# Kernel optimization log

Measured on AMD Instinct MI355X. Metric: run time of the kernel, lower is better.

## Reference

```python
import jax, jax.numpy as jnp
import numpy as np

N_NODES = 32768
N_EDGES = 65536
NODE_IN = 4
EDGE_IN = 4
HIDDEN = 64
LN_EPS = 1e-5


def setup_inputs() -> dict:
    key = jax.random.key(0)
    ks = jax.random.split(key, 20)
    s = 0.05
    inp = {
        "x": jax.random.normal(ks[0], (N_NODES, NODE_IN), dtype=jnp.float32),
        "edge_attr": jax.random.normal(ks[1], (N_EDGES, EDGE_IN), dtype=jnp.float32),
        "edge_index": jax.random.randint(ks[2], (2, N_EDGES), 0, N_NODES, dtype=jnp.int64),
        "batch": jnp.zeros((N_NODES,), dtype=jnp.int64),
        # layer 1: edge MLP edge_in->64->node_in*hidden, root [node_in,hidden]
        "e1_w1": jax.random.normal(ks[3], (EDGE_IN, 64), dtype=jnp.float32) * s,
        "e1_b1": jnp.zeros((64,), jnp.float32),
        "e1_w2": jax.random.normal(ks[4], (64, NODE_IN * HIDDEN), dtype=jnp.float32) * s,
        "e1_b2": jnp.zeros((NODE_IN * HIDDEN,), jnp.float32),
        "root1": jax.random.normal(ks[5], (NODE_IN, HIDDEN), dtype=jnp.float32) * s,
        "bias1": jnp.zeros((HIDDEN,), jnp.float32),
        "ln1_g": jnp.ones((HIDDEN,), jnp.float32),
        "ln1_b": jnp.zeros((HIDDEN,), jnp.float32),
        # layer 2: edge MLP edge_in->128->hidden*hidden, root [hidden,hidden]
        "e2_w1": jax.random.normal(ks[6], (EDGE_IN, 128), dtype=jnp.float32) * s,
        "e2_b1": jnp.zeros((128,), jnp.float32),
        "e2_w2": jax.random.normal(ks[7], (128, HIDDEN * HIDDEN), dtype=jnp.float32) * s,
        "e2_b2": jnp.zeros((HIDDEN * HIDDEN,), jnp.float32),
        "root2": jax.random.normal(ks[8], (HIDDEN, HIDDEN), dtype=jnp.float32) * s,
        "bias2": jnp.zeros((HIDDEN,), jnp.float32),
        "ln2_g": jnp.ones((HIDDEN,), jnp.float32),
        "ln2_b": jnp.zeros((HIDDEN,), jnp.float32),
    }
    return inp


def _nnconv(x, src, dst, edge_attr, ew1, eb1, ew2, eb2, root, bias, n_nodes):
    # edge-conditioned weights: [E, in_ch, out_ch]
    in_ch = x.shape[1]
    out_ch = root.shape[1]
    h = jax.nn.relu(edge_attr @ ew1 + eb1) @ ew2 + eb2
    W = h.reshape(-1, in_ch, out_ch)
    # gather source features, per-edge matvec, scatter-mean to dest
    msg = jnp.einsum('ei,eio->eo', x[src], W)  # [E, out_ch]
    summed = jax.ops.segment_sum(msg, dst, num_segments=n_nodes)
    cnt = jax.ops.segment_sum(jnp.ones((dst.shape[0],), msg.dtype), dst,
                              num_segments=n_nodes)
    agg = summed / jnp.maximum(cnt, 1.0)[:, None]
    return agg + x @ root + bias


def _layernorm(x, g, b):
    m = x.mean(-1, keepdims=True)
    v = ((x - m) ** 2).mean(-1, keepdims=True)
    return (x - m) * jax.lax.rsqrt(v + LN_EPS) * g + b


def reference(x, edge_attr, e1_w1, e1_b1, e1_w2, e1_b2, root1, bias1, ln1_g, ln1_b,
              e2_w1, e2_b1, e2_w2, e2_b2, root2, bias2, ln2_g, ln2_b,
              edge_index, batch):
    src, dst = edge_index[0], edge_index[1]
    n = x.shape[0]
    h = _nnconv(x, src, dst, edge_attr, e1_w1, e1_b1, e1_w2, e1_b2, root1, bias1, n)
    h = _layernorm(jax.nn.relu(h), ln1_g, ln1_b)  # dropout = identity (eval)
    h = _nnconv(h, src, dst, edge_attr, e2_w1, e2_b1, e2_w2, e2_b2, root2, bias2, n)
    h = _layernorm(jax.nn.relu(h), ln2_g, ln2_b)
    # global mean pool (single graph -> [1, hidden])
    gs = jax.ops.segment_sum(h, batch, num_segments=1)
    gc = jax.ops.segment_sum(jnp.ones((n,), h.dtype), batch, num_segments=1)
    return gs / jnp.maximum(gc, 1.0)[:, None]
```

## Files before the change

### kernel.cpp

```cpp
#include <hip/hip_runtime.h>

#define N_NODES 32768
#define N_EDGES 65536

typedef float f32x4 __attribute__((ext_vector_type(4)));
typedef short s16x8 __attribute__((ext_vector_type(8)));

__device__ __forceinline__ unsigned short f2bf(float f){
  unsigned u = __float_as_uint(f);
  u += 0x7FFFu + ((u >> 16) & 1u);
  return (unsigned short)(u >> 16);
}
__device__ __forceinline__ float bf2f(unsigned short b){
  return __uint_as_float(((unsigned)b) << 16);
}

__global__ void k_prep(const float* __restrict__ e2_w2, const float* __restrict__ e2_b2,
                       const float* __restrict__ e1_w2,
                       unsigned short* __restrict__ W2f, unsigned short* __restrict__ T1g,
                       int* __restrict__ cz){
  int idx = blockIdx.x * 256 + threadIdx.x;
  if (idx < 129 * 4096){
    int j = idx & 7, l = (idx >> 3) & 63, half = (idx >> 9) & 1, ot = (idx >> 10) & 3, kf = idx >> 12;
    int i = half * 32 + ((l >> 4) << 3) + j;
    int o = ot * 16 + (l & 15);
    float v = (kf < 128) ? e2_w2[kf * 4096 + i * 64 + o] : e2_b2[i * 64 + o];
    W2f[idx] = f2bf(v);
  } else if (idx < 129 * 4096 + 16384){
    int t = idx - 129 * 4096;
    int j = t & 7, l = (t >> 3) & 63, half = (t >> 9) & 1, ot = (t >> 10) & 3, i = t >> 12;
    int kf = half * 32 + ((l >> 4) << 3) + j;
    int o = ot * 16 + (l & 15);
    T1g[t] = f2bf(e1_w2[kf * 256 + i * 64 + o]);
  } else {
    int z = idx - (129 * 4096 + 16384);
    if (z < 65536) cz[z] = 0;
  }
}

__global__ void k_hist(const int* __restrict__ ei, int* __restrict__ cnti){
  int i = blockIdx.x * 256 + threadIdx.x;
  if (i < N_EDGES) atomicAdd(cnti + ei[N_EDGES + i], 1);
}

__global__ void k_scanA(const int* __restrict__ cnti, int* __restrict__ lex, int* __restrict__ bsum){
  const int tid = threadIdx.x;
  int n = blockIdx.x * 256 + tid;
  int c = cnti[n];
  int v = c;
  int lane = tid & 63;
  #pragma unroll
  for (int d = 1; d < 64; d <<= 1){
    int t = __shfl_up(v, d);
    if (lane >= d) v += t;
  }
  __shared__ int wsum[4];
  if (lane == 63) wsum[tid >> 6] = v;
  __syncthreads();
  int off = 0;
  for (int i = 0; i < (tid >> 6); ++i) off += wsum[i];
  lex[n] = off + v - c;
  if (tid == 255) bsum[blockIdx.x] = off + v;
}

__global__ void k_scanB(const int* __restrict__ bsum, int* __restrict__ bsx){
  const int tid = threadIdx.x;
  int c = bsum[tid];
  int v = c;
  int lane = tid & 63;
  #pragma unroll
  for (int d = 1; d < 64; d <<= 1){
    int t = __shfl_up(v, d);
    if (lane >= d) v += t;
  }
  __shared__ int w0;
  if (tid == 63) w0 = v;
  __syncthreads();
  if (tid >= 64) v += w0;
  bsx[tid] = v - c;
}

__global__ void k_fill(const int* __restrict__ ei, const int* __restrict__ lex,
                       const int* __restrict__ bsx, int* __restrict__ cur,
                       int* __restrict__ eslot){
  int e = blockIdx.x * 256 + threadIdx.x;
  if (e < N_EDGES){
    int d = ei[N_EDGES + e];
    int base = lex[d] + bsx[d >> 8];
    eslot[e] = base + atomicAdd(cur + d, 1);
  }
}

__launch_bounds__(256, 4)
__global__ void k_msg1(const float* __restrict__ x, const float* __restrict__ ea,
                       const int* __restrict__ ei, const int* __restrict__ eslot,
                       const float* __restrict__ e1_w1, const float* __restrict__ e1_b1,
                       const float* __restrict__ e1_b2,
                       const unsigned short* __restrict__ T1g,
                       float* __restrict__ msg)
{
  __shared__ float eas[64 * 4];
  __shared__ unsigned short F1f[8 * 64 * 8];
  const int tid = threadIdx.x;
  const int eblk = blockIdx.x * 64;

  if (tid < 64) ((float4*)eas)[tid] = ((const float4*)ea)[eblk + tid];
  __syncthreads();
  {
    int kf = tid & 63, eh = tid >> 6;
    float w0 = e1_w1[kf], w1 = e1_w1[64 + kf], w2 = e1_w1[128 + kf], w3 = e1_w1[192 + kf];
    float bb = e1_b1[kf];
    int half = kf >> 5, hi = (kf >> 3) & 3, j = kf & 7;
    for (int e = eh * 16; e < eh * 16 + 16; ++e){
      float s = fmaf(eas[e*4+0], w0, fmaf(eas[e*4+1], w1, fmaf(eas[e*4+2], w2, fmaf(eas[e*4+3], w3, bb))));
      F1f[(((e >> 4) * 2 + half) * 64 + hi * 16 + (e & 15)) * 8 + j] = f2bf(fmaxf(s, 0.f));
    }
  }
  __syncthreads();

  const int l = tid & 63, lm = l & 15, lg = l >> 4;
  const int ot = tid >> 6;
  int esl[4];
  float xs[4][4];
  s16x8 bf[4][2];
  #pragma unroll
  for (int et = 0; et < 4; ++et){
    int e = eblk + et * 16 + lm;
    int s = ei[e];
    esl[et] = eslot[e];
    float4 xv = *(const float4*)(x + s * 4);
    xs[et][0] = xv.x; xs[et][1] = xv.y; xs[et][2] = xv.z; xs[et][3] = xv.w;
    bf[et][0] = ((const s16x8*)F1f)[(et * 2 + 0) * 64 + l];
    bf[et][1] = ((const s16x8*)F1f)[(et * 2 + 1) * 64 + l];
  }
  f32x4 acc[4];
  #pragma unroll
  for (int et = 0; et < 4; ++et) acc[et] = (f32x4){0.f, 0.f, 0.f, 0.f};

  #pragma unroll
  for (int i = 0; i < 4; ++i){
    const s16x8* p = (const s16x8*)(T1g + (i * 4 + ot) * 1024);
    s16x8 a0 = p[l], a1 = p[64 + l];
    #pragma unroll
    for (int et = 0; et < 4; ++et){
      f32x4 g = (f32x4){0.f, 0.f, 0.f, 0.f};
      g = __builtin_amdgcn_mfma_f32_16x16x32_bf16(a0, bf[et][0], g, 0, 0, 0);
      g = __builtin_amdgcn_mfma_f32_16x16x32_bf16(a1, bf[et][1], g, 0, 0, 0);
      acc[et] += xs[et][i] * g;
    }
  }
  float b2v[4][4];
  #pragma unroll
  for (int i = 0; i < 4; ++i)
    #pragma unroll
    for (int r = 0; r < 4; ++r) b2v[i][r] = e1_b2[i * 64 + ot * 16 + lg * 4 + r];
  #pragma unroll
  for (int et = 0; et < 4; ++et)
    #pragma unroll
    for (int r = 0; r < 4; ++r)
      #pragma unroll
      for (int i = 0; i < 4; ++i) acc[et][r] = fmaf(xs[et][i], b2v[i][r], acc[et][r]);

  #pragma unroll
  for (int et = 0; et < 4; ++et)
    *(f32x4*)(msg + (size_t)esl[et] * 64 + ot * 16 + lg * 4) = acc[et];
}

__launch_bounds__(256)
__global__ void k_node1(const float* __restrict__ x, const float* __restrict__ root1,
                        const float* __restrict__ bias1, const float* __restrict__ lng,
                        const float* __restrict__ lnb, const int* __restrict__ cnti,
                        const int* __restrict__ lex, const int* __restrict__ bsx,
                        const float* __restrict__ msg, unsigned short* __restrict__ h1b)
{
  const int tid = threadIdx.x;
  int n = blockIdx.x * 4 + (tid >> 6);
  int o = tid & 63;
  int rp = lex[n] + bsx[n >> 8];
  int deg = cnti[n];
  float s = 0.f;
  for (int j = 0; j < deg; ++j) s += msg[(size_t)(rp + j) * 64 + o];
  float v = s * (1.f / fmaxf((float)deg, 1.f));
  float4 xv = *(const float4*)(x + n * 4);
  v = fmaf(xv.x, root1[o], v);
  v = fmaf(xv.y, root1[64 + o], v);
  v = fmaf(xv.z, root1[128 + o], v);
  v = fmaf(xv.w, root1[192 + o], v);
  v = fmaxf(v + bias1[o], 0.f);
  float m = v;
  #pragma unroll
  for (int d = 32; d > 0; d >>= 1) m += __shfl_xor(m, d);
  m *= (1.f / 64.f);
  float dd = v - m;
  float var = dd * dd;
  #pragma unroll
  for (int d = 32; d > 0; d >>= 1) var += __shfl_xor(var, d);
  var *= (1.f / 64.f);
  float out = dd * rsqrtf(var + 1e-5f) * lng[o] + lnb[o];
  h1b[n * 64 + o] = f2bf(out);
}

__launch_bounds__(512, 4)
__global__ void k_msg2(const float* __restrict__ ea, const int* __restrict__ ei,
                       const int* __restrict__ eslot,
                       const float* __restrict__ e2_w1, const float* __restrict__ e2_b1,
                       const unsigned short* __restrict__ h1b,
                       const unsigned short* __restrict__ W2f,
                       float* __restrict__ msg)
{
  __shared__ float eas[128 * 4];
  __shared__ float F2s[128 * 132];
  const int tid = threadIdx.x;
  const int eblk = blockIdx.x * 128;
  const int w = tid >> 6, l = tid & 63, lm = l & 15, lg = l >> 4;
  const int ot = w >> 1, eh = w & 1;

  int esl[4];
  s16x8 bh[4][2];
  #pragma unroll
  for (int et = 0; et < 4; ++et){
    int eloc = eh * 64 + et * 16 + lm;
    int e = eblk + eloc;
    int s = ei[e];
    esl[et] = eslot[e];
    const s16x8* hp = (const s16x8*)(h1b + s * 64);
    bh[et][0] = hp[lg];
    bh[et][1] = hp[4 + lg];
  }

  if (tid < 128) ((float4*)eas)[tid] = ((const float4*)ea)[eblk + tid];
  __syncthreads();
  {
    int kf = tid & 127, q = tid >> 7;
    float w0 = e2_w1[kf], w1 = e2_w1[128 + kf], w2 = e2_w1[256 + kf], w3 = e2_w1[384 + kf];
    float bb = e2_b1[kf];
    for (int e = q * 32; e < q * 32 + 32; ++e){
      float s = fmaf(eas[e*4+0], w0, fmaf(eas[e*4+1], w1, fmaf(eas[e*4+2], w2, fmaf(eas[e*4+3], w3, bb))));
      F2s[e * 132 + kf] = fmaxf(s, 0.f);
    }
  }
  __syncthreads();

  f32x4 acc[4];
  #pragma unroll
  for (int et = 0; et < 4; ++et) acc[et] = (f32x4){0.f, 0.f, 0.f, 0.f};

  const int voff = ot * 2048 + l * 16;
  s16x8 A0[2], A1[2], A2[2], A3[2];

#define LOADA(DST, KF) { \
    const unsigned short* sb = W2f + (size_t)(KF) * 4096; \
    asm volatile("global_load_dwordx4 %0, %2, %3\n\t" \
                 "global_load_dwordx4 %1, %2, %3 offset:1024" \
      : "=&v"(DST[0]), "=&v"(DST[1]) : "v"(voff), "s"(sb)); }
#define WAITA(N) do { asm volatile("s_waitcnt vmcnt(" #N ")"); \
                      __builtin_amdgcn_sched_barrier(0); } while(0);
#define STEP(A, J) { \
    _Pragma("unroll") \
    for (int et = 0; et < 4; ++et){ \
      f32x4 g = (f32x4){0.f, 0.f, 0.f, 0.f}; \
      g = __builtin_amdgcn_mfma_f32_16x16x32_bf16(A[0], bh[et][0], g, 0, 0, 0); \
      g = __builtin_amdgcn_mfma_f32_16x16x32_bf16(A[1], bh[et][1], g, 0, 0, 0); \
      acc[et] += f2c[et][J] * g; \
    } }

  LOADA(A0, 0)
  LOADA(A1, 1)
  LOADA(A2, 2)
  LOADA(A3, 3)
  #pragma unroll 1
  for (int kf = 0; kf < 128; kf += 4){
    f32x4 f2c[4];
    #pragma unroll
    for (int et = 0; et < 4; ++et)
      f2c[et] = *(const f32x4*)&F2s[(eh * 64 + et * 16 + lm) * 132 + kf];
    const int k5 = (kf + 5 > 128) ? 128 : kf + 5;
    const int k6 = (kf + 6 > 128) ? 128 : kf + 6;
    const int k7 = (kf + 7 > 128) ? 128 : kf + 7;
    WAITA(6) STEP(A0, 0) LOADA(A0, kf + 4)
    WAITA(6) STEP(A1, 1) LOADA(A1, k5)
    WAITA(6) STEP(A2, 2) LOADA(A2, k6)
    WAITA(6) STEP(A3, 3) LOADA(A3, k7)
  }
  WAITA(0)
  #pragma unroll
  for (int et = 0; et < 4; ++et){
    acc[et] = __builtin_amdgcn_mfma_f32_16x16x32_bf16(A0[0], bh[et][0], acc[et], 0, 0, 0);
    acc[et] = __builtin_amdgcn_mfma_f32_16x16x32_bf16(A0[1], bh[et][1], acc[et], 0, 0, 0);
  }
#undef LOADA
#undef WAITA
#undef STEP

  #pragma unroll
  for (int et = 0; et < 4; ++et)
    *(f32x4*)(msg + (size_t)esl[et] * 64 + ot * 16 + lg * 4) = acc[et];
}

__launch_bounds__(1024)
__global__ void k_node2(const unsigned short* __restrict__ h1b, const float* __restrict__ root2,
                        const float* __restrict__ bias2, const float* __restrict__ lng,
                        const float* __restrict__ lnb, const int* __restrict__ cnti,
                        const int* __restrict__ lex, const int* __restrict__ bsx,
                        const float* __restrict__ msg, float* __restrict__ partial)
{
  const int tid = threadIdx.x;
  const int q = tid >> 6, o = tid & 63;
  float tsum = 0.f;
  #pragma unroll 1
  for (int it = 0; it < 4; ++it){
    int n = blockIdx.x * 64 + it * 16 + q;
    int rp = lex[n] + bsx[n >> 8];
    int deg = cnti[n];
    float s = 0.f;
    for (int j = 0; j < deg; ++j) s += msg[(size_t)(rp + j) * 64 + o];
    float v = s * (1.f / fmaxf((float)deg, 1.f));
    const s16x8* hp = (const s16x8*)(h1b + n * 64);
    #pragma unroll
    for (int c = 0; c < 8; ++c){
      s16x8 hv = hp[c];
      #pragma unroll
      for (int j = 0; j < 8; ++j)
        v = fmaf(bf2f((unsigned short)hv[j]), root2[(c * 8 + j) * 64 + o], v);
    }
    v = fmaxf(v + bias2[o], 0.f);
    float m = v;
    #pragma unroll
    for (int d = 32; d > 0; d >>= 1) m += __shfl_xor(m, d);
    m *= (1.f / 64.f);
    float dd = v - m;
    float var = dd * dd;
    #pragma unroll
    for (int d = 32; d > 0; d >>= 1) var += __shfl_xor(var, d);
    var *= (1.f / 64.f);
    tsum += dd * rsqrtf(var + 1e-5f) * lng[o] + lnb[o];
  }
  __shared__ float pp[16][64];
  pp[q][o] = tsum;
  __syncthreads();
  if (tid < 64){
    float t = 0.f;
    #pragma unroll
    for (int k = 0; k < 16; ++k) t += pp[k][tid];
    partial[blockIdx.x * 64 + tid] = t;
  }
}

__launch_bounds__(1024)
__global__ void k_out(const float* __restrict__ partial, float* __restrict__ out){
  const int tid = threadIdx.x;
  int o = tid & 63, q = tid >> 6;
  float s = 0.f;
  for (int b = q; b < 512; b += 16) s += partial[b * 64 + o];
  __shared__ float pp[16][64];
  pp[q][o] = s;
  __syncthreads();
  if (tid < 64){
    float t = 0.f;
    #pragma unroll
    for (int k = 0; k < 16; ++k) t += pp[k][tid];
    out[tid] = t * (1.f / 32768.f);
  }
}

extern "C" void kernel_launch(void* const* d_in, const int* in_sizes, int n_in,
                              void* d_out, int out_size, void* d_ws, size_t ws_size,
                              hipStream_t stream)
{
  const float* x      = (const float*)d_in[0];
  const float* ea     = (const float*)d_in[1];
  const int*   ei     = (const int*)  d_in[2];
  const float* e1_w1  = (const float*)d_in[4];
  const float* e1_b1  = (const float*)d_in[5];
  const float* e1_w2  = (const float*)d_in[6];
  const float* e1_b2  = (const float*)d_in[7];
  const float* root1  = (const float*)d_in[8];
  const float* bias1  = (const float*)d_in[9];
  const float* ln1g   = (const float*)d_in[10];
  const float* ln1b   = (const float*)d_in[11];
  const float* e2_w1  = (const float*)d_in[12];
  const float* e2_b1  = (const float*)d_in[13];
  const float* e2_w2  = (const float*)d_in[14];
  const float* e2_b2  = (const float*)d_in[15];
  const float* root2  = (const float*)d_in[16];
  const float* bias2  = (const float*)d_in[17];
  const float* ln2g   = (const float*)d_in[18];
  const float* ln2b   = (const float*)d_in[19];

  char* w = (char*)d_ws;
  float*          msg     = (float*)(w);
  unsigned short* h1b     = (unsigned short*)(w + 16777216);
  unsigned short* W2f     = (unsigned short*)(w + 20971520);
  unsigned short* T1g     = (unsigned short*)(w + 22028288);
  int*            cnti    = (int*)(w + 22061056);
  int*            cur     = (int*)(w + 22192128);
  int*            lex     = (int*)(w + 22323200);
  int*            bsx     = (int*)(w + 22454272);
  int*            bsum    = (int*)(w + 22454784);
  int*            eslot   = (int*)(w + 22455296);
  float*          partial = (float*)(w + 22717440);

  k_prep <<<2384, 256, 0, stream>>>(e2_w2, e2_b2, e1_w2, W2f, T1g, cnti);
  k_hist <<<256, 256, 0, stream>>>(ei, cnti);
  k_scanA<<<128, 256, 0, stream>>>(cnti, lex, bsum);
  k_scanB<<<1, 128, 0, stream>>>(bsum, bsx);
  k_fill <<<256, 256, 0, stream>>>(ei, lex, bsx, cur, eslot);
  k_msg1 <<<1024, 256, 0, stream>>>(x, ea, ei, eslot, e1_w1, e1_b1, e1_b2, T1g, msg);
  k_node1<<<8192, 256, 0, stream>>>(x, root1, bias1, ln1g, ln1b, cnti, lex, bsx, msg, h1b);
  k_msg2 <<<512, 512, 0, stream>>>(ea, ei, eslot, e2_w1, e2_b1, h1b, W2f, msg);
  k_node2<<<512, 1024, 0, stream>>>(h1b, root2, bias2, ln2g, ln2b, cnti, lex, bsx, msg, partial);
  k_out  <<<1, 1024, 0, stream>>>(partial, (float*)d_out);
}
```

Before: 156.0 us.

## Split K across waves in msg2 and store layer-1 messages as bf16

After: 171.7 us. 1.1x slower.

```diff
diff --git a/kernel.cpp b/kernel.cpp
--- a/kernel.cpp
+++ b/kernel.cpp
@@ -5,6 +5,7 @@
 
 typedef float f32x4 __attribute__((ext_vector_type(4)));
 typedef short s16x8 __attribute__((ext_vector_type(8)));
+typedef short s16x4 __attribute__((ext_vector_type(4)));
 
 __device__ __forceinline__ unsigned short f2bf(float f){
   unsigned u = __float_as_uint(f);
@@ -97,7 +98,7 @@
                        const float* __restrict__ e1_w1, const float* __restrict__ e1_b1,
                        const float* __restrict__ e1_b2,
                        const unsigned short* __restrict__ T1g,
-                       float* __restrict__ msg)
+                       unsigned short* __restrict__ msg1b)
 {
   __shared__ float eas[64 * 4];
   __shared__ unsigned short F1f[8 * 64 * 8];
@@ -162,8 +163,11 @@
       for (int i = 0; i < 4; ++i) acc[et][r] = fmaf(xs[et][i], b2v[i][r], acc[et][r]);
 
   #pragma unroll
-  for (int et = 0; et < 4; ++et)
-    *(f32x4*)(msg + (size_t)esl[et] * 64 + ot * 16 + lg * 4) = acc[et];
+  for (int et = 0; et < 4; ++et){
+    unsigned p0 = ((unsigned)f2bf(acc[et][1]) << 16) | f2bf(acc[et][0]);
+    unsigned p1 = ((unsigned)f2bf(acc[et][3]) << 16) | f2bf(acc[et][2]);
+    *(uint2*)(msg1b + (size_t)esl[et] * 64 + ot * 16 + lg * 4) = make_uint2(p0, p1);
+  }
 }
 
 __launch_bounds__(256)
@@ -171,7 +175,7 @@
                         const float* __restrict__ bias1, const float* __restrict__ lng,
                         const float* __restrict__ lnb, const int* __restrict__ cnti,
                         const int* __restrict__ lex, const int* __restrict__ bsx,
-                        const float* __restrict__ msg, unsigned short* __restrict__ h1b)
+                        const unsigned short* __restrict__ msg1b, unsigned short* __restrict__ h1b)
 {
   const int tid = threadIdx.x;
   int n = blockIdx.x * 4 + (tid >> 6);
@@ -179,7 +183,7 @@
   int rp = lex[n] + bsx[n >> 8];
   int deg = cnti[n];
   float s = 0.f;
-  for (int j = 0; j < deg; ++j) s += msg[(size_t)(rp + j) * 64 + o];
+  for (int j = 0; j < deg; ++j) s += bf2f(msg1b[(size_t)(rp + j) * 64 + o]);
   float v = s * (1.f / fmaxf((float)deg, 1.f));
   float4 xv = *(const float4*)(x + n * 4);
   v = fmaf(xv.x, root1[o], v);
@@ -209,23 +213,20 @@
                        float* __restrict__ msg)
 {
   __shared__ float eas[128 * 4];
-  __shared__ float F2s[128 * 132];
+  __shared__ __align__(16) unsigned short F2s[128 * 132];
   const int tid = threadIdx.x;
   const int eblk = blockIdx.x * 128;
   const int w = tid >> 6, l = tid & 63, lm = l & 15, lg = l >> 4;
-  const int ot = w >> 1, eh = w & 1;
-
-  int esl[4];
-  s16x8 bh[4][2];
-  #pragma unroll
-  for (int et = 0; et < 4; ++et){
-    int eloc = eh * 64 + et * 16 + lm;
-    int e = eblk + eloc;
+  const int ot = w >> 1, ki = w & 1;
+
+  int esl[8];
+  s16x8 bh[8];
+  #pragma unroll
+  for (int et = 0; et < 8; ++et){
+    int e = eblk + et * 16 + lm;
     int s = ei[e];
     esl[et] = eslot[e];
-    const s16x8* hp = (const s16x8*)(h1b + s * 64);
-    bh[et][0] = hp[lg];
-    bh[et][1] = hp[4 + lg];
+    bh[et] = ((const s16x8*)(h1b + s * 64))[ki * 4 + lg];
   }
 
   if (tid < 128) ((float4*)eas)[tid] = ((const float4*)ea)[eblk + tid];
@@ -236,32 +237,30 @@
     float bb = e2_b1[kf];
     for (int e = q * 32; e < q * 32 + 32; ++e){
       float s = fmaf(eas[e*4+0], w0, fmaf(eas[e*4+1], w1, fmaf(eas[e*4+2], w2, fmaf(eas[e*4+3], w3, bb))));
-      F2s[e * 132 + kf] = fmaxf(s, 0.f);
+      F2s[e * 132 + kf] = f2bf(fmaxf(s, 0.f));
     }
   }
   __syncthreads();
 
-  f32x4 acc[4];
-  #pragma unroll
-  for (int et = 0; et < 4; ++et) acc[et] = (f32x4){0.f, 0.f, 0.f, 0.f};
-
-  const int voff = ot * 2048 + l * 16;
-  s16x8 A0[2], A1[2], A2[2], A3[2];
+  f32x4 acc[8];
+  #pragma unroll
+  for (int et = 0; et < 8; ++et) acc[et] = (f32x4){0.f, 0.f, 0.f, 0.f};
+
+  const int voff = ot * 2048 + ki * 1024 + l * 16;
+  s16x8 A0, A1, A2, A3;
 
 #define LOADA(DST, KF) { \
     const unsigned short* sb = W2f + (size_t)(KF) * 4096; \
-    asm volatile("global_load_dwordx4 %0, %2, %3\n\t" \
-                 "global_load_dwordx4 %1, %2, %3 offset:1024" \
-      : "=&v"(DST[0]), "=&v"(DST[1]) : "v"(voff), "s"(sb)); }
+    asm volatile("global_load_dwordx4 %0, %1, %2" \
+      : "=&v"(DST) : "v"(voff), "s"(sb)); }
 #define WAITA(N) do { asm volatile("s_waitcnt vmcnt(" #N ")"); \
                       __builtin_amdgcn_sched_barrier(0); } while(0);
 #define STEP(A, J) { \
     _Pragma("unroll") \
-    for (int et = 0; et < 4; ++et){ \
+    for (int et = 0; et < 8; ++et){ \
       f32x4 g = (f32x4){0.f, 0.f, 0.f, 0.f}; \
-      g = __builtin_amdgcn_mfma_f32_16x16x32_bf16(A[0], bh[et][0], g, 0, 0, 0); \
-      g = __builtin_amdgcn_mfma_f32_16x16x32_bf16(A[1], bh[et][1], g, 0, 0, 0); \
-      acc[et] += f2c[et][J] * g; \
+      g = __builtin_amdgcn_mfma_f32_16x16x32_bf16(A, bh[et], g, 0, 0, 0); \
+      acc[et] += bf2f((unsigned short)f2c[et][J]) * g; \
     } }
 
   LOADA(A0, 0)
@@ -270,31 +269,41 @@
   LOADA(A3, 3)
   #pragma unroll 1
   for (int kf = 0; kf < 128; kf += 4){
-    f32x4 f2c[4];
-    #pragma unroll
-    for (int et = 0; et < 4; ++et)
-      f2c[et] = *(const f32x4*)&F2s[(eh * 64 + et * 16 + lm) * 132 + kf];
+    s16x4 f2c[8];
+    #pragma unroll
+    for (int et = 0; et < 8; ++et)
+      f2c[et] = *(const s16x4*)&F2s[(et * 16 + lm) * 132 + kf];
     const int k5 = (kf + 5 > 128) ? 128 : kf + 5;
     const int k6 = (kf + 6 > 128) ? 128 : kf + 6;
     const int k7 = (kf + 7 > 128) ? 128 : kf + 7;
-    WAITA(6) STEP(A0, 0) LOADA(A0, kf + 4)
-    WAITA(6) STEP(A1, 1) LOADA(A1, k5)
-    WAITA(6) STEP(A2, 2) LOADA(A2, k6)
-    WAITA(6) STEP(A3, 3) LOADA(A3, k7)
+    WAITA(3) STEP(A0, 0) LOADA(A0, kf + 4)
+    WAITA(3) STEP(A1, 1) LOADA(A1, k5)
+    WAITA(3) STEP(A2, 2) LOADA(A2, k6)
+    WAITA(3) STEP(A3, 3) LOADA(A3, k7)
   }
   WAITA(0)
   #pragma unroll
-  for (int et = 0; et < 4; ++et){
-    acc[et] = __builtin_amdgcn_mfma_f32_16x16x32_bf16(A0[0], bh[et][0], acc[et], 0, 0, 0);
-    acc[et] = __builtin_amdgcn_mfma_f32_16x16x32_bf16(A0[1], bh[et][1], acc[et], 0, 0, 0);
-  }
+  for (int et = 0; et < 8; ++et)
+    acc[et] = __builtin_amdgcn_mfma_f32_16x16x32_bf16(A0, bh[et], acc[et], 0, 0, 0);
 #undef LOADA
 #undef WAITA
 #undef STEP
 
-  #pragma unroll
-  for (int et = 0; et < 4; ++et)
-    *(f32x4*)(msg + (size_t)esl[et] * 64 + ot * 16 + lg * 4) = acc[et];
+  __syncthreads();
+  float* red = (float*)F2s;
+  if (ki == 1){
+    #pragma unroll
+    for (int et = 0; et < 8; ++et)
+      *(f32x4*)&red[((ot * 8 + et) * 64 + l) * 4] = acc[et];
+  }
+  __syncthreads();
+  if (ki == 0){
+    #pragma unroll
+    for (int et = 0; et < 8; ++et){
+      acc[et] += *(const f32x4*)&red[((ot * 8 + et) * 64 + l) * 4];
+      *(f32x4*)(msg + (size_t)esl[et] * 64 + ot * 16 + lg * 4) = acc[et];
+    }
+  }
 }
 
 __launch_bounds__(1024)
@@ -389,6 +398,7 @@
 
   char* w = (char*)d_ws;
   float*          msg     = (float*)(w);
+  unsigned short* msg1b   = (unsigned short*)(w);
   unsigned short* h1b     = (unsigned short*)(w + 16777216);
   unsigned short* W2f     = (unsigned short*)(w + 20971520);
   unsigned short* T1g     = (unsigned short*)(w + 22028288);
@@ -405,8 +415,8 @@
   k_scanA<<<128, 256, 0, stream>>>(cnti, lex, bsum);
   k_scanB<<<1, 128, 0, stream>>>(bsum, bsx);
   k_fill <<<256, 256, 0, stream>>>(ei, lex, bsx, cur, eslot);
-  k_msg1 <<<1024, 256, 0, stream>>>(x, ea, ei, eslot, e1_w1, e1_b1, e1_b2, T1g, msg);
-  k_node1<<<8192, 256, 0, stream>>>(x, root1, bias1, ln1g, ln1b, cnti, lex, bsx, msg, h1b);
+  k_msg1 <<<1024, 256, 0, stream>>>(x, ea, ei, eslot, e1_w1, e1_b1, e1_b2, T1g, msg1b);
+  k_node1<<<8192, 256, 0, stream>>>(x, root1, bias1, ln1g, ln1b, cnti, lex, bsx, msg1b, h1b);
   k_msg2 <<<512, 512, 0, stream>>>(ea, ei, eslot, e2_w1, e2_b1, h1b, W2f, msg);
   k_node2<<<512, 1024, 0, stream>>>(h1b, root2, bias2, ln2g, ln2b, cnti, lex, bsx, msg, partial);
   k_out  <<<1, 1024, 0, stream>>>(partial, (float*)d_out);
```

## Store edge messages in bf16, stage weight prep through LDS, raise MFMA priority

Applied to the files above, without the earlier changes.

New measurement: 155.2 us. Within noise of the previous version (-0.5%).

```diff
diff --git a/kernel.cpp b/kernel.cpp
--- a/kernel.cpp
+++ b/kernel.cpp
@@ -19,21 +19,29 @@
                        const float* __restrict__ e1_w2,
                        unsigned short* __restrict__ W2f, unsigned short* __restrict__ T1g,
                        int* __restrict__ cz){
-  int idx = blockIdx.x * 256 + threadIdx.x;
-  if (idx < 129 * 4096){
-    int j = idx & 7, l = (idx >> 3) & 63, half = (idx >> 9) & 1, ot = (idx >> 10) & 3, kf = idx >> 12;
-    int i = half * 32 + ((l >> 4) << 3) + j;
-    int o = ot * 16 + (l & 15);
-    float v = (kf < 128) ? e2_w2[kf * 4096 + i * 64 + o] : e2_b2[i * 64 + o];
-    W2f[idx] = f2bf(v);
-  } else if (idx < 129 * 4096 + 16384){
-    int t = idx - 129 * 4096;
+  __shared__ float S[4096];
+  const int b = blockIdx.x, tid = threadIdx.x;
+  if (b < 129){
+    const float* src = (b < 128) ? (e2_w2 + b * 4096) : e2_b2;
+    #pragma unroll
+    for (int t = 0; t < 4096; t += 256) S[t + tid] = src[t + tid];
+    __syncthreads();
+    #pragma unroll
+    for (int t = 0; t < 4096; t += 256){
+      int u = t + tid;
+      int j = u & 7, l = (u >> 3) & 63, half = (u >> 9) & 1, ot = (u >> 10) & 3;
+      int i = half * 32 + ((l >> 4) << 3) + j;
+      int o = ot * 16 + (l & 15);
+      W2f[b * 4096 + u] = f2bf(S[i * 64 + o]);
+    }
+  } else if (b < 193){
+    int t = (b - 129) * 256 + tid;
     int j = t & 7, l = (t >> 3) & 63, half = (t >> 9) & 1, ot = (t >> 10) & 3, i = t >> 12;
     int kf = half * 32 + ((l >> 4) << 3) + j;
     int o = ot * 16 + (l & 15);
     T1g[t] = f2bf(e1_w2[kf * 256 + i * 64 + o]);
   } else {
-    int z = idx - (129 * 4096 + 16384);
+    int z = (b - 193) * 256 + tid;
     if (z < 65536) cz[z] = 0;
   }
 }
@@ -97,7 +105,7 @@
                        const float* __restrict__ e1_w1, const float* __restrict__ e1_b1,
                        const float* __restrict__ e1_b2,
                        const unsigned short* __restrict__ T1g,
-                       float* __restrict__ msg)
+                       unsigned short* __restrict__ msg1b)
 {
   __shared__ float eas[64 * 4];
   __shared__ unsigned short F1f[8 * 64 * 8];
@@ -162,8 +170,11 @@
       for (int i = 0; i < 4; ++i) acc[et][r] = fmaf(xs[et][i], b2v[i][r], acc[et][r]);
 
   #pragma unroll
-  for (int et = 0; et < 4; ++et)
-    *(f32x4*)(msg + (size_t)esl[et] * 64 + ot * 16 + lg * 4) = acc[et];
+  for (int et = 0; et < 4; ++et){
+    unsigned p0 = ((unsigned)f2bf(acc[et][1]) << 16) | f2bf(acc[et][0]);
+    unsigned p1 = ((unsigned)f2bf(acc[et][3]) << 16) | f2bf(acc[et][2]);
+    *(uint2*)(msg1b + (size_t)esl[et] * 64 + ot * 16 + lg * 4) = make_uint2(p0, p1);
+  }
 }
 
 __launch_bounds__(256)
@@ -171,7 +182,7 @@
                         const float* __restrict__ bias1, const float* __restrict__ lng,
                         const float* __restrict__ lnb, const int* __restrict__ cnti,
                         const int* __restrict__ lex, const int* __restrict__ bsx,
-                        const float* __restrict__ msg, unsigned short* __restrict__ h1b)
+                        const unsigned short* __restrict__ msg1b, unsigned short* __restrict__ h1b)
 {
   const int tid = threadIdx.x;
   int n = blockIdx.x * 4 + (tid >> 6);
@@ -179,7 +190,7 @@
   int rp = lex[n] + bsx[n >> 8];
   int deg = cnti[n];
   float s = 0.f;
-  for (int j = 0; j < deg; ++j) s += msg[(size_t)(rp + j) * 64 + o];
+  for (int j = 0; j < deg; ++j) s += bf2f(msg1b[(size_t)(rp + j) * 64 + o]);
   float v = s * (1.f / fmaxf((float)deg, 1.f));
   float4 xv = *(const float4*)(x + n * 4);
   v = fmaf(xv.x, root1[o], v);
@@ -206,7 +217,7 @@
                        const float* __restrict__ e2_w1, const float* __restrict__ e2_b1,
                        const unsigned short* __restrict__ h1b,
                        const unsigned short* __restrict__ W2f,
-                       float* __restrict__ msg)
+                       unsigned short* __restrict__ msgb)
 {
   __shared__ float eas[128 * 4];
   __shared__ float F2s[128 * 132];
@@ -256,13 +267,15 @@
 #define WAITA(N) do { asm volatile("s_waitcnt vmcnt(" #N ")"); \
                       __builtin_amdgcn_sched_barrier(0); } while(0);
 #define STEP(A, J) { \
+    __builtin_amdgcn_s_setprio(1); \
     _Pragma("unroll") \
     for (int et = 0; et < 4; ++et){ \
       f32x4 g = (f32x4){0.f, 0.f, 0.f, 0.f}; \
       g = __builtin_amdgcn_mfma_f32_16x16x32_bf16(A[0], bh[et][0], g, 0, 0, 0); \
       g = __builtin_amdgcn_mfma_f32_16x16x32_bf16(A[1], bh[et][1], g, 0, 0, 0); \
       acc[et] += f2c[et][J] * g; \
-    } }
+    } \
+    __builtin_amdgcn_s_setprio(0); }
 
   LOADA(A0, 0)
   LOADA(A1, 1)
@@ -293,8 +306,11 @@
 #undef STEP
 
   #pragma unroll
-  for (int et = 0; et < 4; ++et)
-    *(f32x4*)(msg + (size_t)esl[et] * 64 + ot * 16 + lg * 4) = acc[et];
+  for (int et = 0; et < 4; ++et){
+    unsigned p0 = ((unsigned)f2bf(acc[et][1]) << 16) | f2bf(acc[et][0]);
+    unsigned p1 = ((unsigned)f2bf(acc[et][3]) << 16) | f2bf(acc[et][2]);
+    *(uint2*)(msgb + (size_t)esl[et] * 64 + ot * 16 + lg * 4) = make_uint2(p0, p1);
+  }
 }
 
 __launch_bounds__(1024)
@@ -302,7 +318,7 @@
                         const float* __restrict__ bias2, const float* __restrict__ lng,
                         const float* __restrict__ lnb, const int* __restrict__ cnti,
                         const int* __restrict__ lex, const int* __restrict__ bsx,
-                        const float* __restrict__ msg, float* __restrict__ partial)
+                        const unsigned short* __restrict__ msgb, float* __restrict__ partial)
 {
   const int tid = threadIdx.x;
   const int q = tid >> 6, o = tid & 63;
@@ -313,7 +329,7 @@
     int rp = lex[n] + bsx[n >> 8];
     int deg = cnti[n];
     float s = 0.f;
-    for (int j = 0; j < deg; ++j) s += msg[(size_t)(rp + j) * 64 + o];
+    for (int j = 0; j < deg; ++j) s += bf2f(msgb[(size_t)(rp + j) * 64 + o]);
     float v = s * (1.f / fmaxf((float)deg, 1.f));
     const s16x8* hp = (const s16x8*)(h1b + n * 64);
     #pragma unroll
@@ -388,26 +404,26 @@
   const float* ln2b   = (const float*)d_in[19];
 
   char* w = (char*)d_ws;
-  float*          msg     = (float*)(w);
-  unsigned short* h1b     = (unsigned short*)(w + 16777216);
-  unsigned short* W2f     = (unsigned short*)(w + 20971520);
-  unsigned short* T1g     = (unsigned short*)(w + 22028288);
-  int*            cnti    = (int*)(w + 22061056);
-  int*            cur     = (int*)(w + 22192128);
-  int*            lex     = (int*)(w + 22323200);
-  int*            bsx     = (int*)(w + 22454272);
-  int*            bsum    = (int*)(w + 22454784);
-  int*            eslot   = (int*)(w + 22455296);
-  float*          partial = (float*)(w + 22717440);
-
-  k_prep <<<2384, 256, 0, stream>>>(e2_w2, e2_b2, e1_w2, W2f, T1g, cnti);
+  unsigned short* msgb    = (unsigned short*)(w);
+  unsigned short* h1b     = (unsigned short*)(w + 8388608);
+  unsigned short* W2f     = (unsigned short*)(w + 12582912);
+  unsigned short* T1g     = (unsigned short*)(w + 13639680);
+  int*            cnti    = (int*)(w + 13672448);
+  int*            cur     = (int*)(w + 13803520);
+  int*            lex     = (int*)(w + 13934592);
+  int*            bsx     = (int*)(w + 14065664);
+  int*            bsum    = (int*)(w + 14066176);
+  int*            eslot   = (int*)(w + 14066688);
+  float*          partial = (float*)(w + 14328832);
+
+  k_prep <<<449, 256, 0, stream>>>(e2_w2, e2_b2, e1_w2, W2f, T1g, cnti);
   k_hist <<<256, 256, 0, stream>>>(ei, cnti);
   k_scanA<<<128, 256, 0, stream>>>(cnti, lex, bsum);
   k_scanB<<<1, 128, 0, stream>>>(bsum, bsx);
   k_fill <<<256, 256, 0, stream>>>(ei, lex, bsx, cur, eslot);
-  k_msg1 <<<1024, 256, 0, stream>>>(x, ea, ei, eslot, e1_w1, e1_b1, e1_b2, T1g, msg);
-  k_node1<<<8192, 256, 0, stream>>>(x, root1, bias1, ln1g, ln1b, cnti, lex, bsx, msg, h1b);
-  k_msg2 <<<512, 512, 0, stream>>>(ea, ei, eslot, e2_w1, e2_b1, h1b, W2f, msg);
-  k_node2<<<512, 1024, 0, stream>>>(h1b, root2, bias2, ln2g, ln2b, cnti, lex, bsx, msg, partial);
+  k_msg1 <<<1024, 256, 0, stream>>>(x, ea, ei, eslot, e1_w1, e1_b1, e1_b2, T1g, msgb);
+  k_node1<<<8192, 256, 0, stream>>>(x, root1, bias1, ln1g, ln1b, cnti, lex, bsx, msgb, h1b);
+  k_msg2 <<<512, 512, 0, stream>>>(ea, ei, eslot, e2_w1, e2_b1, h1b, W2f, msgb);
+  k_node2<<<512, 1024, 0, stream>>>(h1b, root2, bias2, ln2g, ln2b, cnti, lex, bsx, msgb, partial);
   k_out  <<<1, 1024, 0, stream>>>(partial, (float*)d_out);
 }
```
